# Kernel optimization log

Measured on AMD Instinct MI355X. Metric: run time of the kernel, lower is better.

Reference implementation:

```python
import jax, jax.numpy as jnp
import numpy as np

EMBED = 128
HEADS = 8
HEAD_DIM = EMBED // HEADS

def setup_inputs() -> dict:
    key = jax.random.key(0)
    ks = jax.random.split(key, 8)
    B, N = 2, 4096
    values = jax.random.normal(ks[0], (B, N, EMBED), dtype=jnp.float32)
    keys = jax.random.normal(ks[1], (B, N, EMBED), dtype=jnp.float32)
    query = jax.random.normal(ks[2], (B, N, EMBED), dtype=jnp.float32)
    s = 1.0 / np.sqrt(HEAD_DIM)
    Wv = jax.random.normal(ks[3], (HEAD_DIM, HEAD_DIM), dtype=jnp.float32) * s
    Wk = jax.random.normal(ks[4], (HEAD_DIM, HEAD_DIM), dtype=jnp.float32) * s
    Wq = jax.random.normal(ks[5], (HEAD_DIM, HEAD_DIM), dtype=jnp.float32) * s
    Wo = jax.random.normal(ks[6], (EMBED, EMBED), dtype=jnp.float32) * (1.0 / np.sqrt(EMBED))
    bo = jnp.zeros((EMBED,), dtype=jnp.float32)
    return {"values": values, "keys": keys, "query": query,
            "Wv": Wv, "Wk": Wk, "Wq": Wq, "Wo": Wo, "bo": bo}

def reference(values, keys, query, Wv, Wk, Wq, Wo, bo):
    B, N, _ = query.shape
    # split heads: [B,N,H,Dh]
    v = values.reshape(B, N, HEADS, HEAD_DIM)
    k = keys.reshape(B, N, HEADS, HEAD_DIM)
    q = query.reshape(B, N, HEADS, HEAD_DIM)
    # per-head linear (torch Linear: x @ W.T), same weight for all heads
    v = jnp.einsum('bnhd,ed->bnhe', v, Wv)
    k = jnp.einsum('bnhd,ed->bnhe', k, Wk)
    q = jnp.einsum('bnhd,ed->bnhe', q, Wq)
    # scores [B,H,N,N], note scale by sqrt(embed_size) as in original
    energy = jnp.einsum('bqhd,bkhd->bhqk', q, k) / jnp.sqrt(jnp.float32(EMBED))
    attn = jax.nn.softmax(energy, axis=-1)
    out = jnp.einsum('bhql,blhd->bqhd', attn, v).reshape(B, N, EMBED)
    return out @ Wo.T + bo
```

## Files before the change

kernel.cpp:

```cpp
#include <hip/hip_runtime.h>

#define BB 2
#define NN 4096
#define HH 8
#define DD 16
#define EE 128
#define LBLK 128
#define NSPL 4
#define NIV 4

typedef _Float16 f16;
typedef _Float16 f16x4 __attribute__((ext_vector_type(4)));
typedef _Float16 f16x2 __attribute__((ext_vector_type(2)));
typedef _Float16 f16x8 __attribute__((ext_vector_type(8)));
typedef __fp16 h16x2 __attribute__((ext_vector_type(2)));
typedef float f32x4 __attribute__((ext_vector_type(4)));

#define QSCALE 0.12751741f

__global__ __launch_bounds__(256) void proj_kernel(
    const float* __restrict__ vals, const float* __restrict__ keys,
    const float* __restrict__ query,
    const float* __restrict__ Wv, const float* __restrict__ Wk,
    const float* __restrict__ Wq, const float* __restrict__ Wo,
    f16* __restrict__ Qp, f16* __restrict__ Kp, f16* __restrict__ Vt,
    f16* __restrict__ Wo16)
{
    if (blockIdx.x >= 768) {
        const int i = (blockIdx.x - 768) * 256 + threadIdx.x;
        Wo16[i] = (f16)Wo[i];
        return;
    }
    __shared__ float W[256];
    const int p = blockIdx.x >> 8;
    const float* Wsrc = (p == 0) ? Wv : ((p == 1) ? Wk : Wq);
    W[threadIdx.x] = Wsrc[threadIdx.x];
    __syncthreads();

    const int idx = ((blockIdx.x & 255) << 8) | threadIdx.x;
    const int n = idx & 4095;
    const int h = (idx >> 12) & 7;
    const int b = idx >> 15;

    const float* xsrc = (p == 0) ? vals : ((p == 1) ? keys : query);
    const float4* xp = (const float4*)(xsrc + (size_t)(b * NN + n) * EE + h * DD);
    const float4 x0 = xp[0], x1 = xp[1], x2 = xp[2], x3 = xp[3];
    const float scale = (p == 2) ? QSCALE : 1.0f;

    alignas(16) f16 out[16];
    #pragma unroll
    for (int e = 0; e < 16; e++) {
        const float4* wr = (const float4*)(W + e * 16);
        const float4 w0 = wr[0], w1 = wr[1], w2 = wr[2], w3 = wr[3];
        float acc = x0.x * w0.x + x0.y * w0.y + x0.z * w0.z + x0.w * w0.w
                  + x1.x * w1.x + x1.y * w1.y + x1.z * w1.z + x1.w * w1.w
                  + x2.x * w2.x + x2.y * w2.y + x2.z * w2.z + x2.w * w2.w
                  + x3.x * w3.x + x3.y * w3.y + x3.z * w3.z + x3.w * w3.w;
        out[e] = (f16)(acc * scale);
    }

    if (p == 0) {
        f16* dst = Vt + (size_t)(b * HH + h) * DD * NN + n;
        #pragma unroll
        for (int e = 0; e < 16; e++) dst[(size_t)e * NN] = out[e];
    } else {
        f16* dst = ((p == 1) ? Kp : Qp) + (size_t)((b * HH + h) * NN + n) * DD;
        ((uint4*)dst)[0] = ((const uint4*)out)[0];
        ((uint4*)dst)[1] = ((const uint4*)out)[1];
    }
}

__global__ __launch_bounds__(512, 8) void attn_kernel(
    const f16* __restrict__ Qp, const f16* __restrict__ Kp,
    const f16* __restrict__ Vt, float* __restrict__ Oacc,
    float* __restrict__ den)
{
    __shared__ alignas(16) f16 Kl[2][2][2048];
    __shared__ alignas(16) f16 Vl[2][2][2048];

    const int tid = threadIdx.x;
    const int lane = tid & 63;
    const int wave = tid >> 6;
    const int r = lane & 15;
    const int g = lane >> 4;

    const int bid = blockIdx.x;
    const int quarter = bid & 3;
    const int qt = (bid >> 2) & 15;
    const int bh = bid >> 6;
    const int q0 = qt * 256 + wave * 32;
    const int L0 = quarter * (NN / NSPL);

    const int ti = tid >> 8;
    const int u = tid & 255;
    const bool isK = u < 128;
    const f16* gbase;
    int w0, w1;
    if (isK) {
        const int spair = u >> 6;
        const int lp = u & 63;
        const int rr = lp & 15, gg = lp >> 4;
        const int lam = 8 * (rr >> 2) + (rr & 3);
        gbase = Kp + ((size_t)bh * NN + L0 + ti * LBLK + 64 * spair + lam) * DD + 4 * gg;
        w0 = (2 * spair) * 512 + lp * 8;
        w1 = (2 * spair + 1) * 512 + lp * 8;
    } else {
        const int v = u - 128;
        gbase = Vt + ((size_t)bh * DD + (v & 15)) * NN + L0 + ti * LBLK
                   + 32 * (v >> 6) + 8 * ((v >> 4) & 3);
        w0 = v * 8;
        w1 = 1024 + v * 8;
    }
    const size_t gstep = isK ? (size_t)(2 * LBLK) * DD : (size_t)(2 * LBLK);

    const f16x4 qf0 = *(const f16x4*)(Qp + ((size_t)bh * NN + q0 + r) * DD + 4 * g);
    const f16x4 qf1 = *(const f16x4*)(Qp + ((size_t)bh * NN + q0 + 16 + r) * DD + 4 * g);

    f16x8 sA, sB;
#define STAGE_LOAD() { \
    if (isK) { \
        const f16x4 a0 = *(const f16x4*)(gbase + 0); \
        const f16x4 a1 = *(const f16x4*)(gbase + 64); \
        const f16x4 a2 = *(const f16x4*)(gbase + 512); \
        const f16x4 a3 = *(const f16x4*)(gbase + 576); \
        sA = __builtin_shufflevector(a0, a1, 0,1,2,3,4,5,6,7); \
        sB = __builtin_shufflevector(a2, a3, 0,1,2,3,4,5,6,7); \
    } else { \
        sA = *(const f16x8*)(gbase + 0); \
        sB = *(const f16x8*)(gbase + 64); \
    } \
    gbase += gstep; }

#define STAGE_WRITE(HALF) { \
    f16* wp = isK ? &Kl[HALF][ti][0] : &Vl[HALF][ti][0]; \
    *(f16x8*)(wp + w0) = sA; \
    *(f16x8*)(wp + w1) = sB; }

    STAGE_LOAD();
    STAGE_WRITE(0);
    __syncthreads();

    f32x4 acc0 = {0.f,0.f,0.f,0.f}, acc1 = {0.f,0.f,0.f,0.f};
    f32x4 dacc0 = {0.f,0.f,0.f,0.f}, dacc1 = {0.f,0.f,0.f,0.f};
    const f32x4 zz = {0.f,0.f,0.f,0.f};
    const f16x8 ones8 = {(f16)1.f,(f16)1.f,(f16)1.f,(f16)1.f,
                         (f16)1.f,(f16)1.f,(f16)1.f,(f16)1.f};

#define QKPV(QF, ACC, DACC) { \
    const f32x4 st0 = __builtin_amdgcn_mfma_f32_16x16x16f16(kfA, (QF), zz, 0, 0, 0); \
    const f32x4 st1 = __builtin_amdgcn_mfma_f32_16x16x16f16(kfB, (QF), zz, 0, 0, 0); \
    const float e0 = __builtin_amdgcn_exp2f(st0[0]); \
    const float e1 = __builtin_amdgcn_exp2f(st0[1]); \
    const float e2 = __builtin_amdgcn_exp2f(st0[2]); \
    const float e3 = __builtin_amdgcn_exp2f(st0[3]); \
    const float f0 = __builtin_amdgcn_exp2f(st1[0]); \
    const float f1 = __builtin_amdgcn_exp2f(st1[1]); \
    const float f2 = __builtin_amdgcn_exp2f(st1[2]); \
    const float f3 = __builtin_amdgcn_exp2f(st1[3]); \
    const h16x2 h0 = __builtin_amdgcn_cvt_pkrtz(e0, e1); \
    const h16x2 h1 = __builtin_amdgcn_cvt_pkrtz(e2, e3); \
    const h16x2 h2 = __builtin_amdgcn_cvt_pkrtz(f0, f1); \
    const h16x2 h3 = __builtin_amdgcn_cvt_pkrtz(f2, f3); \
    const f16x4 pA = __builtin_shufflevector( \
        __builtin_bit_cast(f16x2, h0), __builtin_bit_cast(f16x2, h1), 0, 1, 2, 3); \
    const f16x4 pB = __builtin_shufflevector( \
        __builtin_bit_cast(f16x2, h2), __builtin_bit_cast(f16x2, h3), 0, 1, 2, 3); \
    const f16x8 pf8 = __builtin_shufflevector(pA, pB, 0, 1, 2, 3, 4, 5, 6, 7); \
    ACC  = __builtin_amdgcn_mfma_f32_16x16x32_f16(vf8, pf8, ACC, 0, 0, 0); \
    DACC = __builtin_amdgcn_mfma_f32_16x16x32_f16(ones8, pf8, DACC, 0, 0, 0); }

    int half = 0;
    for (int iv = 0; iv < NIV; ++iv) {
        if (iv < NIV - 1) STAGE_LOAD();

        #pragma unroll
        for (int t2 = 0; t2 < 2; ++t2) {
            const f16* Kb = &Kl[half][t2][0];
            const f16* Vb = &Vl[half][t2][0];
            #pragma unroll
            for (int s = 0; s < 4; ++s) {
                const f16x8 kf8 = *(const f16x8*)(Kb + s * 512 + lane * 8);
                const f16x8 vf8 = *(const f16x8*)(Vb + s * 512 + lane * 8);
                const f16x4 kfA = __builtin_shufflevector(kf8, kf8, 0, 1, 2, 3);
                const f16x4 kfB = __builtin_shufflevector(kf8, kf8, 4, 5, 6, 7);
                QKPV(qf0, acc0, dacc0)
                QKPV(qf1, acc1, dacc1)
            }
        }

        if (iv < NIV - 1) STAGE_WRITE(half ^ 1);
        __syncthreads();
        half ^= 1;
    }
#undef QKPV
#undef STAGE_WRITE
#undef STAGE_LOAD

    const int b = bh >> 3, h = bh & 7;
    float* OaccQ = Oacc + (size_t)quarter * (BB * NN * EE);
    *(f32x4*)(OaccQ + ((size_t)(b * NN + q0 + r)) * EE + h * DD + 4 * g) = acc0;
    *(f32x4*)(OaccQ + ((size_t)(b * NN + q0 + 16 + r)) * EE + h * DD + 4 * g) = acc1;
    if (lane < 16) {
        den[(size_t)(quarter * 16 + bh) * NN + q0 + lane] = dacc0[0];
        den[(size_t)(quarter * 16 + bh) * NN + q0 + 16 + lane] = dacc1[0];
    }
}

__global__ __launch_bounds__(256) void outproj_kernel(
    const float* __restrict__ Oacc, const float* __restrict__ den,
    const f16* __restrict__ Wo16, const float* __restrict__ bo,
    float* __restrict__ out)
{
    const int lane = threadIdx.x & 63;
    const int wave = threadIdx.x >> 6;
    const int r = lane & 15;
    const int g = lane >> 4;
    const int n0 = (blockIdx.x * 2 + (wave >> 1)) * 16;
    const int eh = (wave & 1) * 4;

    const int n = n0 + r;
    const int b = n >> 12;
    const int nn = n & 4095;
    const float* Oa0 = Oacc + (size_t)n * EE;
    const float* Oa1 = Oa0 + (size_t)1 * (BB * NN * EE);
    const float* Oa2 = Oa0 + (size_t)2 * (BB * NN * EE);
    const float* Oa3 = Oa0 + (size_t)3 * (BB * NN * EE);

    f32x4 acc[4];
    #pragma unroll
    for (int e = 0; e < 4; e++) acc[e] = (f32x4){0.f, 0.f, 0.f, 0.f};

    #pragma unroll
    for (int k0 = 0; k0 < 8; k0++) {
        const size_t didx = (size_t)(b * 8 + k0) * NN + nn;
        const float inv = 1.0f / ((den[didx] + den[(size_t)16 * NN + didx])
                                + (den[(size_t)32 * NN + didx] + den[(size_t)48 * NN + didx]));
        const f32x4 xa = *(const f32x4*)(Oa0 + k0 * 16 + 4 * g)
                       + *(const f32x4*)(Oa1 + k0 * 16 + 4 * g)
                       + *(const f32x4*)(Oa2 + k0 * 16 + 4 * g)
                       + *(const f32x4*)(Oa3 + k0 * 16 + 4 * g);
        const float s0 = xa[0] * inv;
        const float s1 = xa[1] * inv;
        const float s2 = xa[2] * inv;
        const float s3 = xa[3] * inv;
        const f16x4 a = __builtin_shufflevector(
            __builtin_bit_cast(f16x2, __builtin_amdgcn_cvt_pkrtz(s0, s1)),
            __builtin_bit_cast(f16x2, __builtin_amdgcn_cvt_pkrtz(s2, s3)), 0, 1, 2, 3);
        #pragma unroll
        for (int e = 0; e < 4; e++) {
            const f16x4 bf = *(const f16x4*)(Wo16 + (size_t)((eh + e) * 16 + r) * EE + k0 * 16 + 4 * g);
            acc[e] = __builtin_amdgcn_mfma_f32_16x16x16f16(a, bf, acc[e], 0, 0, 0);
        }
    }

    #pragma unroll
    for (int e = 0; e < 4; e++) {
        const float bias = bo[(eh + e) * 16 + r];
        #pragma unroll
        for (int i = 0; i < 4; i++) {
            out[(size_t)(n0 + 4 * g + i) * EE + (eh + e) * 16 + r] = acc[e][i] + bias;
        }
    }
}

extern "C" void kernel_launch(void* const* d_in, const int* in_sizes, int n_in,
                              void* d_out, int out_size, void* d_ws, size_t ws_size,
                              hipStream_t stream)
{
    const float* vals  = (const float*)d_in[0];
    const float* keys  = (const float*)d_in[1];
    const float* query = (const float*)d_in[2];
    const float* Wv    = (const float*)d_in[3];
    const float* Wk    = (const float*)d_in[4];
    const float* Wq    = (const float*)d_in[5];
    const float* Wo    = (const float*)d_in[6];
    const float* bo    = (const float*)d_in[7];
    float* out = (float*)d_out;

    char* w = (char*)d_ws;
    f16*   Qp   = (f16*)(w);
    f16*   Kp   = (f16*)(w + (2u << 20));
    f16*   Vt   = (f16*)(w + (4u << 20));
    f16*   Wo16 = (f16*)(w + (6u << 20));
    float* den  = (float*)(w + (6u << 20) + 65536);
    float* Oacc = (float*)(w + (8u << 20));

    hipLaunchKernelGGL(proj_kernel, dim3(832), dim3(256), 0, stream,
                       vals, keys, query, Wv, Wk, Wq, Wo, Qp, Kp, Vt, Wo16);
    hipLaunchKernelGGL(attn_kernel, dim3(1024), dim3(512), 0, stream,
                       Qp, Kp, Vt, Oacc, den);
    hipLaunchKernelGGL(outproj_kernel, dim3(256), dim3(256), 0, stream,
                       Oacc, den, Wo16, bo, out);
}
```

Measured before the change: 54.33 us.

## Store partial attention outputs in fp16, reorder block mapping, raise MFMA wave priority

The split-K partial attention accumulators (Oacc) are now converted to fp16 before being stored, and the output projection reads them back as fp16 and widens to fp32. This halves the intermediate traffic between the attention and output-projection kernels. Block index decoding is also swapped so consecutive blocks share a query tile across different heads, and s_setprio raises wave priority around the MFMA compute loop. The fp16 partials are unnormalized sums and could lose precision or overflow for large values.

```diff
diff --git a/kernel.cpp b/kernel.cpp
--- a/kernel.cpp
+++ b/kernel.cpp
@@ -72,7 +72,7 @@
 
 __global__ __launch_bounds__(512, 8) void attn_kernel(
     const f16* __restrict__ Qp, const f16* __restrict__ Kp,
-    const f16* __restrict__ Vt, float* __restrict__ Oacc,
+    const f16* __restrict__ Vt, f16* __restrict__ Oacc,
     float* __restrict__ den)
 {
     __shared__ alignas(16) f16 Kl[2][2][2048];
@@ -86,8 +86,8 @@
 
     const int bid = blockIdx.x;
     const int quarter = bid & 3;
-    const int qt = (bid >> 2) & 15;
-    const int bh = bid >> 6;
+    const int bh = (bid >> 2) & 15;
+    const int qt = bid >> 6;
     const int q0 = qt * 256 + wave * 32;
     const int L0 = quarter * (NN / NSPL);
 
@@ -173,6 +173,7 @@
     for (int iv = 0; iv < NIV; ++iv) {
         if (iv < NIV - 1) STAGE_LOAD();
 
+        __builtin_amdgcn_s_setprio(1);
         #pragma unroll
         for (int t2 = 0; t2 < 2; ++t2) {
             const f16* Kb = &Kl[half][t2][0];
@@ -187,6 +188,7 @@
                 QKPV(qf1, acc1, dacc1)
             }
         }
+        __builtin_amdgcn_s_setprio(0);
 
         if (iv < NIV - 1) STAGE_WRITE(half ^ 1);
         __syncthreads();
@@ -197,17 +199,27 @@
 #undef STAGE_LOAD
 
     const int b = bh >> 3, h = bh & 7;
-    float* OaccQ = Oacc + (size_t)quarter * (BB * NN * EE);
-    *(f32x4*)(OaccQ + ((size_t)(b * NN + q0 + r)) * EE + h * DD + 4 * g) = acc0;
-    *(f32x4*)(OaccQ + ((size_t)(b * NN + q0 + 16 + r)) * EE + h * DD + 4 * g) = acc1;
+    f16* OaccQ = Oacc + (size_t)quarter * (BB * NN * EE);
+    const f16x4 o0 = __builtin_shufflevector(
+        __builtin_bit_cast(f16x2, __builtin_amdgcn_cvt_pkrtz(acc0[0], acc0[1])),
+        __builtin_bit_cast(f16x2, __builtin_amdgcn_cvt_pkrtz(acc0[2], acc0[3])), 0, 1, 2, 3);
+    const f16x4 o1 = __builtin_shufflevector(
+        __builtin_bit_cast(f16x2, __builtin_amdgcn_cvt_pkrtz(acc1[0], acc1[1])),
+        __builtin_bit_cast(f16x2, __builtin_amdgcn_cvt_pkrtz(acc1[2], acc1[3])), 0, 1, 2, 3);
+    *(f16x4*)(OaccQ + ((size_t)(b * NN + q0 + r)) * EE + h * DD + 4 * g) = o0;
+    *(f16x4*)(OaccQ + ((size_t)(b * NN + q0 + 16 + r)) * EE + h * DD + 4 * g) = o1;
     if (lane < 16) {
         den[(size_t)(quarter * 16 + bh) * NN + q0 + lane] = dacc0[0];
         den[(size_t)(quarter * 16 + bh) * NN + q0 + 16 + lane] = dacc1[0];
     }
 }
 
+static __device__ __forceinline__ f32x4 cvt4(f16x4 x) {
+    return (f32x4){(float)x[0], (float)x[1], (float)x[2], (float)x[3]};
+}
+
 __global__ __launch_bounds__(256) void outproj_kernel(
-    const float* __restrict__ Oacc, const float* __restrict__ den,
+    const f16* __restrict__ Oacc, const float* __restrict__ den,
     const f16* __restrict__ Wo16, const float* __restrict__ bo,
     float* __restrict__ out)
 {
@@ -221,10 +233,10 @@
     const int n = n0 + r;
     const int b = n >> 12;
     const int nn = n & 4095;
-    const float* Oa0 = Oacc + (size_t)n * EE;
-    const float* Oa1 = Oa0 + (size_t)1 * (BB * NN * EE);
-    const float* Oa2 = Oa0 + (size_t)2 * (BB * NN * EE);
-    const float* Oa3 = Oa0 + (size_t)3 * (BB * NN * EE);
+    const f16* Oa0 = Oacc + (size_t)n * EE;
+    const f16* Oa1 = Oa0 + (size_t)1 * (BB * NN * EE);
+    const f16* Oa2 = Oa0 + (size_t)2 * (BB * NN * EE);
+    const f16* Oa3 = Oa0 + (size_t)3 * (BB * NN * EE);
 
     f32x4 acc[4];
     #pragma unroll
@@ -235,10 +247,10 @@
         const size_t didx = (size_t)(b * 8 + k0) * NN + nn;
         const float inv = 1.0f / ((den[didx] + den[(size_t)16 * NN + didx])
                                 + (den[(size_t)32 * NN + didx] + den[(size_t)48 * NN + didx]));
-        const f32x4 xa = *(const f32x4*)(Oa0 + k0 * 16 + 4 * g)
-                       + *(const f32x4*)(Oa1 + k0 * 16 + 4 * g)
-                       + *(const f32x4*)(Oa2 + k0 * 16 + 4 * g)
-                       + *(const f32x4*)(Oa3 + k0 * 16 + 4 * g);
+        const f32x4 xa = (cvt4(*(const f16x4*)(Oa0 + k0 * 16 + 4 * g))
+                        + cvt4(*(const f16x4*)(Oa1 + k0 * 16 + 4 * g)))
+                       + (cvt4(*(const f16x4*)(Oa2 + k0 * 16 + 4 * g))
+                        + cvt4(*(const f16x4*)(Oa3 + k0 * 16 + 4 * g)));
         const float s0 = xa[0] * inv;
         const float s1 = xa[1] * inv;
         const float s2 = xa[2] * inv;
@@ -283,7 +295,7 @@
     f16*   Vt   = (f16*)(w + (4u << 20));
     f16*   Wo16 = (f16*)(w + (6u << 20));
     float* den  = (float*)(w + (6u << 20) + 65536);
-    float* Oacc = (float*)(w + (8u << 20));
+    f16*   Oacc = (f16*)(w + (8u << 20));
 
     hipLaunchKernelGGL(proj_kernel, dim3(832), dim3(256), 0, stream,
                        vals, keys, query, Wv, Wk, Wq, Wo, Qp, Kp, Vt, Wo16);
```

New measurement: 53.69 us, median of 2. Within noise of the previous version (-1.2%).
